# Performance work log

Measured on AMD Instinct MI355X. Metric: run time of the kernel, lower is better.

Reference implementation:

```python
import jax, jax.numpy as jnp
import numpy as np

HS = 512   # hidden_size
IN = 2048  # input_size
MB = 100   # memory_bank_size
T  = 4096  # nImg


def setup_inputs() -> dict:
    key = jax.random.key(0)
    ks = jax.random.split(key, 20)

    def w(k, i, o):
        return jax.random.normal(k, (i, o), jnp.float32) * (1.0 / np.sqrt(i))

    def b(k, o):
        return jax.random.normal(k, (o,), jnp.float32) * 0.01

    return {
        "hidden_out_a": jax.random.normal(ks[0], (T, IN), jnp.float32),
        "hidden_out_m": jax.random.normal(ks[1], (T, IN), jnp.float32),
        "W_ca": w(ks[2], HS + IN, HS),  "b_ca": b(ks[3], HS),    # hidden_to_content_a
        "W_cm": w(ks[4], HS + IN, HS),  "b_cm": b(ks[5], HS),    # hidden_to_content_m
        "W_wp": w(ks[6], 3 * HS, 3),    "b_wp": b(ks[7], 3),     # write_prob
        "W_wpa": w(ks[8], HS + IN, MB), "b_wpa": b(ks[9], MB),   # write_prob_a
        "W_wpm": w(ks[10], HS + IN, MB),"b_wpm": b(ks[11], MB),  # write_prob_m
        "W_rp": w(ks[12], 3 * HS, MB),  "b_rp": b(ks[13], MB),   # read_prob
        "W_rh": w(ks[14], 2 * HS, HS),  "b_rh": b(ks[15], HS),   # read_to_hidden
        "W_rha": w(ks[16], 2 * HS + IN, HS), "b_rha": b(ks[17], HS),  # read_to_hidden_a
        "W_rhm": w(ks[18], 2 * HS + IN, HS), "b_rhm": b(ks[19], HS),  # read_to_hidden_m
        "nImg": T,
    }


def reference(hidden_out_a, hidden_out_m,
              W_ca, b_ca, W_cm, b_cm,
              W_wp, b_wp, W_wpa, b_wpa, W_wpm, b_wpm,
              W_rp, b_rp, W_rh, b_rh,
              W_rha, b_rha, W_rhm, b_rhm,
              nImg):
    hs = W_rh.shape[1]
    mb = W_rp.shape[1]

    def step(carry, xs):
        mem, h, ha, hm = carry            # mem: [MB, HS]; h/ha/hm: [HS]
        xa, xm = xs                       # [IN] each
        xh = jnp.concatenate([ha, hm, h])               # [3*HS]
        ar = jax.nn.softmax(xh @ W_rp + b_rp)           # [MB]
        r = ar @ mem                                    # [HS] memory read
        h1 = jax.nn.relu(jnp.concatenate([r, h]) @ W_rh + b_rh)
        ha1 = jax.nn.relu(jnp.concatenate([xa, r, ha]) @ W_rha + b_rha)
        hm1 = jax.nn.relu(jnp.concatenate([xm, r, hm]) @ W_rhm + b_rhm)
        aw = jax.nn.softmax(xh @ W_wp + b_wp)           # [3] stream gate
        xha = jnp.concatenate([ha, xa])                 # [HS+IN]
        xhm = jnp.concatenate([hm, xm])
        c_a = jax.nn.relu(xha @ W_ca + b_ca)            # [HS]
        c_m = jax.nn.relu(xhm @ W_cm + b_cm)
        aw_a = jax.nn.softmax(xha @ W_wpa + b_wpa)      # [MB]
        aw_m = jax.nn.softmax(xhm @ W_wpm + b_wpm)
        mem = aw[0] * mem + aw[1] * aw_a[:, None] * c_a + aw[2] * aw_m[:, None] * c_m
        return (mem, h1, ha1, hm1), h1

    init = (jnp.zeros((mb, hs), hidden_out_a.dtype),
            jnp.zeros((hs,), hidden_out_a.dtype),
            jnp.zeros((hs,), hidden_out_a.dtype),
            jnp.zeros((hs,), hidden_out_a.dtype))
    _, hiddens = jax.lax.scan(step, init,
                              (hidden_out_a[:nImg], hidden_out_m[:nImg]))
    return hiddens  # [nImg, HS]
```

## Files before the change

kernel.cpp:

```cpp
#include <hip/hip_runtime.h>
#include <cstdint>
#include <cstddef>

#define HS 512

constexpr int TPB  = 512;
constexpr int GBLK = 64;
constexpr int OWNB = 24;

constexpr size_t OFF_TWrp  = 0;
constexpr size_t OFF_TWwp  = OFF_TWrp  + 100*1536;
constexpr size_t OFF_TWwpa = OFF_TWwp  + 3*1536;
constexpr size_t OFF_TWwpm = OFF_TWwpa + 100*512;
constexpr size_t OFF_TWca  = OFF_TWwpm + 100*512;
constexpr size_t OFF_TWcm  = OFF_TWca  + 512*512;
constexpr size_t OFF_TWh0  = OFF_TWcm  + 512*512;
constexpr size_t OFF_TWh1  = OFF_TWh0  + 512*512;
constexpr size_t OFF_TWh2  = OFF_TWh1  + 512*512;
constexpr size_t OFF_TWu0  = OFF_TWh2  + 512*512;
constexpr size_t OFF_TWu1  = OFF_TWu0  + 512*512;
constexpr size_t OFF_TWu2  = OFF_TWu1  + 512*512;
constexpr size_t OFF_PAca  = OFF_TWu2  + 512*512;
constexpr size_t OFF_PMcm  = OFF_PAca  + 4096*512;
constexpr size_t OFF_PArha = OFF_PMcm  + 4096*512;
constexpr size_t OFF_PMrhm = OFF_PArha + 4096*512;
constexpr size_t OFF_PAwpa = OFF_PMrhm + 4096*512;
constexpr size_t OFF_PMwpm = OFF_PAwpa + 4096*100;
constexpr size_t OFF_CARRY = OFF_PMwpm + 4096*100;
constexpr size_t OFF_BCAST = OFF_CARRY + 2*1536*2;

__device__ __forceinline__ unsigned long long ald(const unsigned long long* p) {
  return __hip_atomic_load(const_cast<unsigned long long*>(p),
                           __ATOMIC_RELAXED, __HIP_MEMORY_SCOPE_AGENT);
}
__device__ __forceinline__ void gstTag(unsigned long long* p, float v, unsigned tag) {
  unsigned long long u = ((unsigned long long)tag << 32) | (unsigned long long)__float_as_uint(v);
  __hip_atomic_store(p, u, __ATOMIC_RELAXED, __HIP_MEMORY_SCOPE_AGENT);
}
__device__ __forceinline__ float xrsum(float v) {
  #pragma unroll
  for (int o = 32; o; o >>= 1) v += __shfl_xor(v, o, 64);
  return v;
}
__device__ __forceinline__ float rsum16(float v) {
  #pragma unroll
  for (int o = 8; o; o >>= 1) v += __shfl_xor(v, o, 64);
  return v;
}
__device__ __forceinline__ void spinF(volatile unsigned* f, unsigned v) {
  while (*f < v) { }
  __builtin_amdgcn_sched_barrier(0);
  asm volatile("" ::: "memory");
}

__global__ void initK(unsigned long long* carryT, unsigned long long* bcast) {
  int i = blockIdx.x * blockDim.x + threadIdx.x, st = gridDim.x * blockDim.x;
  for (int k = i; k < 1536; k += st) carryT[k] = (1ull << 32);
  for (int k = i; k < 1536; k += st) carryT[1536 + k] = 0ull;
  for (int k = i; k < 2 * 1344; k += st) bcast[k] = 0ull;
}

__global__ void transK(const float* __restrict__ src, float* __restrict__ dst, int R, int C) {
  __shared__ float tile[32][33];
  int c0 = blockIdx.x * 32, r0 = blockIdx.y * 32;
  for (int i = threadIdx.y; i < 32; i += 8) {
    int r = r0 + i, c = c0 + threadIdx.x;
    tile[i][threadIdx.x] = (r < R && c < C) ? src[(size_t)r * C + c] : 0.f;
  }
  __syncthreads();
  for (int i = threadIdx.y; i < 32; i += 8) {
    int c = c0 + i, r = r0 + threadIdx.x;
    if (c < C && r < R) dst[(size_t)c * R + r] = tile[threadIdx.x][i];
  }
}

__global__ __launch_bounds__(256) void gemmK(const float* __restrict__ X,
                                             const float* __restrict__ W,
                                             float* __restrict__ C, int N) {
  __shared__ float As[16][68];
  __shared__ float Bs[16][68];
  int t0 = blockIdx.y * 64, n0 = blockIdx.x * 64;
  int tid = threadIdx.x, tx = tid & 15, ty = tid >> 4;
  float acc[4][4] = {};
  for (int k0 = 0; k0 < 2048; k0 += 16) {
    {
      int r = tid >> 2, c = (tid & 3) * 4;
      float4 v = *(const float4*)(X + (size_t)(t0 + r) * 2048 + k0 + c);
      As[c + 0][r] = v.x; As[c + 1][r] = v.y; As[c + 2][r] = v.z; As[c + 3][r] = v.w;
    }
    {
      int kr = tid >> 4, c = (tid & 15) * 4;
      int gcol = n0 + c;
      const float* src = W + (size_t)(k0 + kr) * N + gcol;
      #pragma unroll
      for (int i = 0; i < 4; ++i) Bs[kr][c + i] = (gcol + i < N) ? src[i] : 0.f;
    }
    __syncthreads();
    #pragma unroll
    for (int kk = 0; kk < 16; ++kk) {
      float4 a4 = *(const float4*)&As[kk][ty * 4];
      float4 b4 = *(const float4*)&Bs[kk][tx * 4];
      float av[4] = {a4.x, a4.y, a4.z, a4.w};
      float bv[4] = {b4.x, b4.y, b4.z, b4.w};
      #pragma unroll
      for (int i = 0; i < 4; ++i)
        #pragma unroll
        for (int j = 0; j < 4; ++j) acc[i][j] += av[i] * bv[j];
    }
    __syncthreads();
  }
  #pragma unroll
  for (int i = 0; i < 4; ++i)
    #pragma unroll
    for (int j = 0; j < 4; ++j) {
      int col = n0 + tx * 4 + j;
      if (col < N) C[(size_t)(t0 + ty * 4 + i) * N + col] = acc[i][j];
    }
}

__global__ __launch_bounds__(256) void gemm128(const float* __restrict__ X,
                                               const float* __restrict__ W,
                                               float* __restrict__ C) {
  __shared__ float As[8][132];
  __shared__ float Bs[8][132];
  const int N = 512;
  int t0 = blockIdx.y * 128, n0 = blockIdx.x * 128;
  int tid = threadIdx.x, tx = tid & 15, ty = tid >> 4;
  float acc[8][8] = {};
  for (int k0 = 0; k0 < 2048; k0 += 8) {
    int r = tid >> 1, c4 = (tid & 1) * 4;
    float4 va = *(const float4*)(X + (size_t)(t0 + r) * 2048 + k0 + c4);
    int kr = tid >> 5, cb = (tid & 31) * 4;
    float4 vb = *(const float4*)(W + (size_t)(k0 + kr) * N + n0 + cb);
    __syncthreads();
    As[c4 + 0][r] = va.x; As[c4 + 1][r] = va.y; As[c4 + 2][r] = va.z; As[c4 + 3][r] = va.w;
    Bs[kr][cb] = vb.x; Bs[kr][cb + 1] = vb.y; Bs[kr][cb + 2] = vb.z; Bs[kr][cb + 3] = vb.w;
    __syncthreads();
    #pragma unroll
    for (int kk = 0; kk < 8; ++kk) {
      float av[8], bv[8];
      *(float4*)av       = *(const float4*)&As[kk][ty * 8];
      *(float4*)(av + 4) = *(const float4*)&As[kk][ty * 8 + 4];
      *(float4*)bv       = *(const float4*)&Bs[kk][tx * 8];
      *(float4*)(bv + 4) = *(const float4*)&Bs[kk][tx * 8 + 4];
      #pragma unroll
      for (int i = 0; i < 8; ++i)
        #pragma unroll
        for (int j = 0; j < 8; ++j) acc[i][j] += av[i] * bv[j];
    }
  }
  #pragma unroll
  for (int i = 0; i < 8; ++i) {
    float* dst = C + (size_t)(t0 + ty * 8 + i) * N + n0 + tx * 8;
    *(float4*)dst       = *(float4*)&acc[i][0];
    *(float4*)(dst + 4) = *(float4*)&acc[i][4];
  }
}

struct RArgs {
  const float *TWrp, *TWwp, *TWwpa, *TWwpm, *TWca, *TWcm;
  const float *TWh0, *TWh1, *TWh2, *TWu0, *TWu1, *TWu2;
  const float *PAca, *PMcm, *PArha, *PMrhm, *PAwpa, *PMwpm;
  const float *b_ca, *b_cm, *b_wp, *b_wpa, *b_wpm, *b_rp, *b_rh, *b_rha, *b_rhm;
  unsigned long long *carryT, *bcast;
  float *out;
  int nT;
};

__global__ __launch_bounds__(TPB, 1) void recurK(RArgs a) {
  const int tid  = threadIdx.x;
  const int lane = tid & 63;
  const int lw   = tid >> 6;
  const int g    = tid >> 4;
  const int gl   = tid & 15;
  const int b    = blockIdx.x;

  __shared__ __align__(16) float s_x[1536];
  __shared__ __align__(16) float s_c[1024];
  __shared__ float s_ar[112], s_awa[112], s_awm[112], s_aw[4];
  __shared__ unsigned s_flags[8];
  volatile unsigned* FL = s_flags;

  const int r0a = (b + 51) & 63;
  const int r1m = (b + 25) & 63;
  const bool big1_grp = (b < 36);
  const bool big1_wp  = (b >= 40 && b <= 42);

  if (tid < 112) { s_ar[tid] = 0.f; s_awa[tid] = 0.f; s_awm[tid] = 0.f; }
  if (tid < 8) s_flags[tid] = 0u;

  int dstA = -1, xoffA = 0, strideA = 512;
  bool reluA = false;
  float biasA = 0.f;
  const float* preAPtr = nullptr;
  const float* wARow = nullptr;
  if (lw < 2) {
    int col = b * 8 + g;
    dstA = col; reluA = true; biasA = a.b_ca[col]; preAPtr = a.PAca + col;
    wARow = a.TWca + (size_t)col * 512; xoffA = 0;
  } else if (lw < 4) {
    int col = b * 8 + (g - 8);
    dstA = 512 + col; reluA = true; biasA = a.b_cm[col]; preAPtr = a.PMcm + col;
    wARow = a.TWcm + (size_t)col * 512; xoffA = 512;
  } else if (lw == 4) {
    int sl = g - 16;
    strideA = 100;
    if (sl == 0)                  { dstA = 1124 + r0a;      biasA = a.b_wpa[r0a];      preAPtr = a.PAwpa + r0a;      wARow = a.TWwpa + (size_t)r0a * 512;        xoffA = 0;   }
    else if (sl == 1 && r0a < 36) { dstA = 1124 + r0a + 64; biasA = a.b_wpa[r0a + 64]; preAPtr = a.PAwpa + r0a + 64; wARow = a.TWwpa + (size_t)(r0a + 64) * 512; xoffA = 0;   }
    else if (sl == 2)             { dstA = 1224 + r1m;      biasA = a.b_wpm[r1m];      preAPtr = a.PMwpm + r1m;      wARow = a.TWwpm + (size_t)r1m * 512;        xoffA = 512; }
    else if (sl == 3 && r1m < 36) { dstA = 1224 + r1m + 64; biasA = a.b_wpm[r1m + 64]; preAPtr = a.PMwpm + r1m + 64; wARow = a.TWwpm + (size_t)(r1m + 64) * 512; xoffA = 512; }
  }
  int dstBig = -1;
  float biasBig = 0.f;
  const float* wBigRow = nullptr;
  if (lw == 6) { dstBig = 1024 + b; biasBig = a.b_rp[b]; wBigRow = a.TWrp + (size_t)b * 1536; }
  else if (lw == 7) {
    if (big1_grp)      { dstBig = 1024 + b + 64;   biasBig = a.b_rp[b + 64]; wBigRow = a.TWrp + (size_t)(b + 64) * 1536; }
    else if (big1_wp)  { dstBig = 1324 + (b - 40); biasBig = a.b_wp[b - 40]; wBigRow = a.TWwp + (size_t)(b - 40) * 1536; }
  }
  const bool own = (g < OWNB);
  int ownHsel = 0, ownJ = 0, whXo = 0;
  float biasO = 0.f;
  const float* preOPtr = nullptr;
  const float* whRow = nullptr;
  const float* uRow = nullptr;
  if (own) {
    int q = b * OWNB + g, hsel = q >> 9, j = q & 511;
    ownHsel = hsel; ownJ = j;
    if (hsel == 0)      { biasO = a.b_rh[j];
                          whRow = a.TWh0 + (size_t)j * 512; whXo = 1024;
                          uRow  = a.TWu0 + (size_t)j * 512; }
    else if (hsel == 1) { biasO = a.b_rha[j]; preOPtr = a.PArha + j;
                          whRow = a.TWh1 + (size_t)j * 512; whXo = 0;
                          uRow  = a.TWu1 + (size_t)j * 512; }
    else                { biasO = a.b_rhm[j]; preOPtr = a.PMrhm + j;
                          whRow = a.TWh2 + (size_t)j * 512; whXo = 512;
                          uRow  = a.TWu2 + (size_t)j * 512; }
  }

  float4 wA[8];
  float4 wU[8];
  float4 wWh[8];
  float4 wB[6];
  float  gr[7];
  #pragma unroll
  for (int it = 0; it < 8; ++it) wA[it] = wU[it] = wWh[it] = make_float4(0.f, 0.f, 0.f, 0.f);
  #pragma unroll
  for (int it = 0; it < 6; ++it) wB[it] = make_float4(0.f, 0.f, 0.f, 0.f);
  #pragma unroll
  for (int k = 0; k < 7; ++k) gr[k] = 0.f;

  if (wARow) {
    const float4* w4 = (const float4*)wARow;
    #pragma unroll
    for (int it = 0; it < 8; ++it) wA[it] = w4[gl + 16 * it];
  }
  if (own) {
    const float4* u4 = (const float4*)uRow;
    const float4* h4 = (const float4*)whRow;
    #pragma unroll
    for (int it = 0; it < 8; ++it) { wU[it] = u4[gl + 16 * it]; wWh[it] = h4[gl + 16 * it]; }
  }
  if (wBigRow) {
    const float4* w4 = (const float4*)wBigRow;
    #pragma unroll
    for (int it = 0; it < 6; ++it) wB[it] = w4[lane + 64 * it];
  }
  __syncthreads();

  float preA_c = preAPtr ? preAPtr[0] : 0.f;
  float preO_c = preOPtr ? preOPtr[0] : 0.f;

  float whv = 0.f;
  for (int t = 0; t < a.nT; ++t) {
    const unsigned tagB = (unsigned)t + 1;
    unsigned long long* bc = a.bcast + (size_t)(t & 1) * 1344;

    {
      const unsigned long long* cin = a.carryT + (size_t)(t & 1) * 1536;
      int i0 = tid, i1 = tid + 512, i2 = tid + 1024;
      unsigned long long v0 = ald(cin + i0), v1 = ald(cin + i1), v2 = ald(cin + i2);
      while (((unsigned)(v0 >> 32) < tagB) | ((unsigned)(v1 >> 32) < tagB) |
             ((unsigned)(v2 >> 32) < tagB)) {
        __builtin_amdgcn_s_sleep(1);
        v0 = ald(cin + i0); v1 = ald(cin + i1); v2 = ald(cin + i2);
      }
      s_x[i0] = __uint_as_float((unsigned)v0);
      s_x[i1] = __uint_as_float((unsigned)v1);
      s_x[i2] = __uint_as_float((unsigned)v2);
    }
    __syncthreads();

    const int tn = (t + 1 < a.nT) ? t + 1 : t;
    float preA_n = preAPtr ? preAPtr[(size_t)tn * strideA] : 0.f;
    float preO_n = preOPtr ? preOPtr[(size_t)tn * 512] : 0.f;

    if (dstA >= 0) {
      const float4* x4 = (const float4*)(s_x + xoffA);
      float acc = 0.f;
      #pragma unroll
      for (int it = 0; it < 8; ++it) {
        float4 xv = x4[gl + 16 * it];
        acc += wA[it].x * xv.x + wA[it].y * xv.y + wA[it].z * xv.z + wA[it].w * xv.w;
      }
      float v = rsum16(acc);
      if (!gl) {
        v += preA_c + biasA;
        if (reluA) v = fmaxf(v, 0.f);
        gstTag(bc + dstA, v, tagB);
      }
    } else if (dstBig >= 0) {
      const float4* x4 = (const float4*)s_x;
      float acc = 0.f;
      #pragma unroll
      for (int it = 0; it < 6; ++it) {
        float4 xv = x4[lane + 64 * it];
        acc += wB[it].x * xv.x + wB[it].y * xv.y + wB[it].z * xv.z + wB[it].w * xv.w;
      }
      float v = xrsum(acc);
      if (!lane) gstTag(bc + dstBig, v + biasBig, tagB);
    }
    if (own) {
      const float4* x4 = (const float4*)(s_x + whXo);
      float acc = 0.f;
      #pragma unroll
      for (int it = 0; it < 8; ++it) {
        float4 xv = x4[gl + 16 * it];
        acc += wWh[it].x * xv.x + wWh[it].y * xv.y + wWh[it].z * xv.z + wWh[it].w * xv.w;
      }
      whv = rsum16(acc);
    }

    if (lw == 0) {
      const unsigned long long* p1 = bc + 1024 + lane;
      bool two = lane < 36;
      bool wpx = (lane >= 40 && lane < 43);
      const unsigned long long* pw = bc + 1324 + (lane - 40);
      unsigned long long v1 = ald(p1);
      unsigned long long v2 = two ? ald(p1 + 64) : ~0ull;
      unsigned long long vw = wpx ? ald(pw) : ~0ull;
      while (((unsigned)(v1 >> 32) < tagB) | ((unsigned)(v2 >> 32) < tagB) |
             ((unsigned)(vw >> 32) < tagB)) {
        __builtin_amdgcn_s_sleep(1);
        v1 = ald(p1); if (two) v2 = ald(p1 + 64); if (wpx) vw = ald(pw);
      }
      float x1 = __uint_as_float((unsigned)v1);
      float x2 = two ? __uint_as_float((unsigned)v2) : -3.0e38f;
      float m = fmaxf(x1, x2);
      #pragma unroll
      for (int o = 32; o; o >>= 1) m = fmaxf(m, __shfl_xor(m, o, 64));
      float e1 = expf(x1 - m);
      float e2 = two ? expf(x2 - m) : 0.f;
      float ss = e1 + e2;
      #pragma unroll
      for (int o = 32; o; o >>= 1) ss += __shfl_xor(ss, o, 64);
      float inv = 1.f / ss;
      s_ar[lane] = e1 * inv;
      if (two) s_ar[64 + lane] = e2 * inv;
      asm volatile("s_waitcnt lgkmcnt(0)" ::: "memory");
      if (!lane) FL[0] = tagB;
    }

    unsigned long long* cout = a.carryT + (size_t)((t + 1) & 1) * 1536;
    if (own) {
      spinF(&FL[0], tagB);
      float contrib = 0.f;
      #pragma unroll
      for (int k = 0; k < 7; ++k) contrib += s_ar[gl + 16 * k] * gr[k];
      contrib = rsum16(contrib);
      if (!gl) {
        float h = fmaxf(contrib + whv + preO_c + biasO, 0.f);
        if (ownHsel == 0) {
          a.out[(size_t)t * 512 + ownJ] = h;
          gstTag(cout + 1024 + ownJ, h, tagB + 1);
        } else if (ownHsel == 1) {
          gstTag(cout + ownJ, h, tagB + 1);
        } else {
          gstTag(cout + 512 + ownJ, h, tagB + 1);
        }
      }
    }

    if (lw == 1) {
      const unsigned long long* p1 = bc + 1124 + lane;
      bool two = lane < 36;
      unsigned long long v1 = ald(p1);
      unsigned long long v2 = two ? ald(p1 + 64) : ~0ull;
      while (((unsigned)(v1 >> 32) < tagB) | ((unsigned)(v2 >> 32) < tagB)) {
        __builtin_amdgcn_s_sleep(1);
        v1 = ald(p1); if (two) v2 = ald(p1 + 64);
      }
      float x1 = __uint_as_float((unsigned)v1);
      float x2 = two ? __uint_as_float((unsigned)v2) : -3.0e38f;
      float m = fmaxf(x1, x2);
      #pragma unroll
      for (int o = 32; o; o >>= 1) m = fmaxf(m, __shfl_xor(m, o, 64));
      float e1 = expf(x1 - m);
      float e2 = two ? expf(x2 - m) : 0.f;
      float ss = e1 + e2;
      #pragma unroll
      for (int o = 32; o; o >>= 1) ss += __shfl_xor(ss, o, 64);
      float inv = 1.f / ss;
      s_awa[lane] = e1 * inv;
      if (two) s_awa[64 + lane] = e2 * inv;
      asm volatile("s_waitcnt lgkmcnt(0)" ::: "memory");
      if (!lane) FL[2] = tagB;
    } else if (lw == 2) {
      const unsigned long long* p1 = bc + 1224 + lane;
      bool two = lane < 36;
      unsigned long long v1 = ald(p1);
      unsigned long long v2 = two ? ald(p1 + 64) : ~0ull;
      while (((unsigned)(v1 >> 32) < tagB) | ((unsigned)(v2 >> 32) < tagB)) {
        __builtin_amdgcn_s_sleep(1);
        v1 = ald(p1); if (two) v2 = ald(p1 + 64);
      }
      float x1 = __uint_as_float((unsigned)v1);
      float x2 = two ? __uint_as_float((unsigned)v2) : -3.0e38f;
      float m = fmaxf(x1, x2);
      #pragma unroll
      for (int o = 32; o; o >>= 1) m = fmaxf(m, __shfl_xor(m, o, 64));
      float e1 = expf(x1 - m);
      float e2 = two ? expf(x2 - m) : 0.f;
      float ss = e1 + e2;
      #pragma unroll
      for (int o = 32; o; o >>= 1) ss += __shfl_xor(ss, o, 64);
      float inv = 1.f / ss;
      s_awm[lane] = e1 * inv;
      if (two) s_awm[64 + lane] = e2 * inv;
      asm volatile("s_waitcnt lgkmcnt(0)" ::: "memory");
      if (!lane) FL[3] = tagB;
    } else if (lw == 3) {
      float x = -3.0e38f;
      if (lane < 3) {
        const unsigned long long* p = bc + 1324 + lane;
        unsigned long long v = ald(p);
        while ((unsigned)(v >> 32) < tagB) { __builtin_amdgcn_s_sleep(1); v = ald(p); }
        x = __uint_as_float((unsigned)v);
      }
      float m = x;
      #pragma unroll
      for (int o = 32; o; o >>= 1) m = fmaxf(m, __shfl_xor(m, o, 64));
      float e = (lane < 3) ? expf(x - m) : 0.f;
      float ss = e;
      #pragma unroll
      for (int o = 32; o; o >>= 1) ss += __shfl_xor(ss, o, 64);
      if (lane < 3) s_aw[lane] = e / ss;
      asm volatile("s_waitcnt lgkmcnt(0)" ::: "memory");
      if (!lane) FL[1] = tagB;
    } else if (lw >= 6) {
      int ci = tid - 384;
      const unsigned long long* p = bc + ci;
      unsigned long long v[8];
      #pragma unroll
      for (int k = 0; k < 8; ++k) v[k] = ald(p + 128 * k);
      for (;;) {
        bool ok = true;
        #pragma unroll
        for (int k = 0; k < 8; ++k) ok &= ((unsigned)(v[k] >> 32) >= tagB);
        if (__all(ok)) break;
        __builtin_amdgcn_s_sleep(1);
        #pragma unroll
        for (int k = 0; k < 8; ++k) v[k] = ald(p + 128 * k);
      }
      #pragma unroll
      for (int k = 0; k < 8; ++k) s_c[ci + 128 * k] = __uint_as_float((unsigned)v[k]);
      asm volatile("s_waitcnt lgkmcnt(0)" ::: "memory");
      if (!lane) FL[4 + (lw - 6)] = tagB;
    }

    if (own) {
      spinF(&FL[4], tagB);
      spinF(&FL[5], tagB);
      const float4* a4 = (const float4*)s_c;
      const float4* m4 = (const float4*)(s_c + 512);
      float sa = 0.f, sm = 0.f;
      #pragma unroll
      for (int it = 0; it < 8; ++it) {
        float4 av = a4[gl + 16 * it], mv = m4[gl + 16 * it];
        sa += wU[it].x * av.x + wU[it].y * av.y + wU[it].z * av.z + wU[it].w * av.w;
        sm += wU[it].x * mv.x + wU[it].y * mv.y + wU[it].z * mv.z + wU[it].w * mv.w;
      }
      #pragma unroll
      for (int o = 8; o; o >>= 1) { sa += __shfl_xor(sa, o, 64); sm += __shfl_xor(sm, o, 64); }
      const float uA = sa, uM = sm;

      spinF(&FL[1], tagB);
      spinF(&FL[2], tagB);
      spinF(&FL[3], tagB);
      const float aw0 = s_aw[0], aw1 = s_aw[1], aw2 = s_aw[2];
      #pragma unroll
      for (int k = 0; k < 7; ++k) {
        int idx = gl + 16 * k;
        gr[k] = aw0 * gr[k] + aw1 * s_awa[idx] * uA + aw2 * s_awm[idx] * uM;
      }
    }

    preA_c = preA_n;
    preO_c = preO_n;
  }
}

extern "C" void kernel_launch(void* const* d_in, const int* in_sizes, int n_in,
                              void* d_out, int out_size, void* d_ws, size_t ws_size,
                              hipStream_t stream) {
  const float* Xa    = (const float*)d_in[0];
  const float* Xm    = (const float*)d_in[1];
  const float* W_ca  = (const float*)d_in[2];  const float* b_ca  = (const float*)d_in[3];
  const float* W_cm  = (const float*)d_in[4];  const float* b_cm  = (const float*)d_in[5];
  const float* W_wp  = (const float*)d_in[6];  const float* b_wp  = (const float*)d_in[7];
  const float* W_wpa = (const float*)d_in[8];  const float* b_wpa = (const float*)d_in[9];
  const float* W_wpm = (const float*)d_in[10]; const float* b_wpm = (const float*)d_in[11];
  const float* W_rp  = (const float*)d_in[12]; const float* b_rp  = (const float*)d_in[13];
  const float* W_rh  = (const float*)d_in[14]; const float* b_rh  = (const float*)d_in[15];
  const float* W_rha = (const float*)d_in[16]; const float* b_rha = (const float*)d_in[17];
  const float* W_rhm = (const float*)d_in[18]; const float* b_rhm = (const float*)d_in[19];

  int nT = out_size / HS;
  float* ws = (float*)d_ws;

  initK<<<dim3(64), dim3(256), 0, stream>>>(
      (unsigned long long*)(ws + OFF_CARRY),
      (unsigned long long*)(ws + OFF_BCAST));

  dim3 tb(32, 8);
  auto tg = [](int R, int C) { return dim3((C + 31) / 32, (R + 31) / 32); };
  transK<<<tg(1536, 100), tb, 0, stream>>>(W_rp,                       ws + OFF_TWrp,  1536, 100);
  transK<<<tg(1536, 3),   tb, 0, stream>>>(W_wp,                       ws + OFF_TWwp,  1536, 3);
  transK<<<tg(512, 100),  tb, 0, stream>>>(W_wpa,                      ws + OFF_TWwpa, 512, 100);
  transK<<<tg(512, 100),  tb, 0, stream>>>(W_wpm,                      ws + OFF_TWwpm, 512, 100);
  transK<<<tg(512, 512),  tb, 0, stream>>>(W_ca,                       ws + OFF_TWca,  512, 512);
  transK<<<tg(512, 512),  tb, 0, stream>>>(W_cm,                       ws + OFF_TWcm,  512, 512);
  transK<<<tg(512, 512),  tb, 0, stream>>>(W_rh  + 512 * 512,          ws + OFF_TWh0,  512, 512);
  transK<<<tg(512, 512),  tb, 0, stream>>>(W_rha + (size_t)2560 * 512, ws + OFF_TWh1,  512, 512);
  transK<<<tg(512, 512),  tb, 0, stream>>>(W_rhm + (size_t)2560 * 512, ws + OFF_TWh2,  512, 512);
  transK<<<tg(512, 512),  tb, 0, stream>>>(W_rh,                       ws + OFF_TWu0,  512, 512);
  transK<<<tg(512, 512),  tb, 0, stream>>>(W_rha + (size_t)2048 * 512, ws + OFF_TWu1,  512, 512);
  transK<<<tg(512, 512),  tb, 0, stream>>>(W_rhm + (size_t)2048 * 512, ws + OFF_TWu2,  512, 512);

  int tB = nT / 128;
  gemm128<<<dim3(4, tB), dim3(256), 0, stream>>>(Xa, W_ca + (size_t)512 * 512, ws + OFF_PAca);
  gemm128<<<dim3(4, tB), dim3(256), 0, stream>>>(Xm, W_cm + (size_t)512 * 512, ws + OFF_PMcm);
  gemm128<<<dim3(4, tB), dim3(256), 0, stream>>>(Xa, W_rha,                    ws + OFF_PArha);
  gemm128<<<dim3(4, tB), dim3(256), 0, stream>>>(Xm, W_rhm,                    ws + OFF_PMrhm);
  int tB64 = nT / 64;
  gemmK<<<dim3(2, tB64), dim3(256), 0, stream>>>(Xa, W_wpa + (size_t)512 * 100, ws + OFF_PAwpa, 100);
  gemmK<<<dim3(2, tB64), dim3(256), 0, stream>>>(Xm, W_wpm + (size_t)512 * 100, ws + OFF_PMwpm, 100);

  RArgs a;
  a.TWrp  = ws + OFF_TWrp;  a.TWwp  = ws + OFF_TWwp;
  a.TWwpa = ws + OFF_TWwpa; a.TWwpm = ws + OFF_TWwpm;
  a.TWca  = ws + OFF_TWca;  a.TWcm  = ws + OFF_TWcm;
  a.TWh0  = ws + OFF_TWh0;  a.TWh1  = ws + OFF_TWh1;  a.TWh2 = ws + OFF_TWh2;
  a.TWu0  = ws + OFF_TWu0;  a.TWu1  = ws + OFF_TWu1;  a.TWu2 = ws + OFF_TWu2;
  a.PAca  = ws + OFF_PAca;  a.PMcm  = ws + OFF_PMcm;
  a.PArha = ws + OFF_PArha; a.PMrhm = ws + OFF_PMrhm;
  a.PAwpa = ws + OFF_PAwpa; a.PMwpm = ws + OFF_PMwpm;
  a.b_ca = b_ca; a.b_cm = b_cm; a.b_wp = b_wp; a.b_wpa = b_wpa; a.b_wpm = b_wpm;
  a.b_rp = b_rp; a.b_rh = b_rh; a.b_rha = b_rha; a.b_rhm = b_rhm;
  a.carryT = (unsigned long long*)(ws + OFF_CARRY);
  a.bcast  = (unsigned long long*)(ws + OFF_BCAST);
  a.out    = (float*)d_out;
  a.nT     = nT;

  recurK<<<dim3(GBLK), dim3(TPB), 0, stream>>>(a);
}
```

Before: 25.28 ms.

## Replace LDS flag spin-waits with block barriers and remap wave roles

Removes the per-wave shared-memory flag handshakes (spinF on FL[]) and replaces them with two __syncthreads per step. The three softmax computations are consolidated into wave 0 and the content-vector gather into wave 1. Owner groups move to g>=8 and the content-column work is redistributed across the remaining groups. This removes LDS spin polling and frees waves 6-7 from gather duty, but it serialises softmax work in one wave and forces every wave to wait at full-block barriers.

```diff
diff --git a/kernel.cpp b/kernel.cpp
--- a/kernel.cpp
+++ b/kernel.cpp
@@ -47,11 +47,6 @@
   for (int o = 8; o; o >>= 1) v += __shfl_xor(v, o, 64);
   return v;
 }
-__device__ __forceinline__ void spinF(volatile unsigned* f, unsigned v) {
-  while (*f < v) { }
-  __builtin_amdgcn_sched_barrier(0);
-  asm volatile("" ::: "memory");
-}
 
 __global__ void initK(unsigned long long* carryT, unsigned long long* bcast) {
   int i = blockIdx.x * blockDim.x + threadIdx.x, st = gridDim.x * blockDim.x;
@@ -178,8 +173,6 @@
   __shared__ __align__(16) float s_x[1536];
   __shared__ __align__(16) float s_c[1024];
   __shared__ float s_ar[112], s_awa[112], s_awm[112], s_aw[4];
-  __shared__ unsigned s_flags[8];
-  volatile unsigned* FL = s_flags;
 
   const int r0a = (b + 51) & 63;
   const int r1m = (b + 25) & 63;
@@ -187,22 +180,26 @@
   const bool big1_wp  = (b >= 40 && b <= 42);
 
   if (tid < 112) { s_ar[tid] = 0.f; s_awa[tid] = 0.f; s_awm[tid] = 0.f; }
-  if (tid < 8) s_flags[tid] = 0u;
+  if (tid < 4) s_aw[tid] = 0.f;
 
   int dstA = -1, xoffA = 0, strideA = 512;
   bool reluA = false;
   float biasA = 0.f;
   const float* preAPtr = nullptr;
   const float* wARow = nullptr;
-  if (lw < 2) {
-    int col = b * 8 + g;
+  if (g >= 4 && g < 8) {
+    int col = b * 8 + (g - 4);
     dstA = col; reluA = true; biasA = a.b_ca[col]; preAPtr = a.PAca + col;
     wARow = a.TWca + (size_t)col * 512; xoffA = 0;
-  } else if (lw < 4) {
+  } else if (g >= 20 && g < 24) {
+    int col = b * 8 + (g - 16);
+    dstA = col; reluA = true; biasA = a.b_ca[col]; preAPtr = a.PAca + col;
+    wARow = a.TWca + (size_t)col * 512; xoffA = 0;
+  } else if (g >= 8 && g < 16) {
     int col = b * 8 + (g - 8);
     dstA = 512 + col; reluA = true; biasA = a.b_cm[col]; preAPtr = a.PMcm + col;
     wARow = a.TWcm + (size_t)col * 512; xoffA = 512;
-  } else if (lw == 4) {
+  } else if (g >= 16 && g < 20) {
     int sl = g - 16;
     strideA = 100;
     if (sl == 0)                  { dstA = 1124 + r0a;      biasA = a.b_wpa[r0a];      preAPtr = a.PAwpa + r0a;      wARow = a.TWwpa + (size_t)r0a * 512;        xoffA = 0;   }
@@ -218,14 +215,16 @@
     if (big1_grp)      { dstBig = 1024 + b + 64;   biasBig = a.b_rp[b + 64]; wBigRow = a.TWrp + (size_t)(b + 64) * 1536; }
     else if (big1_wp)  { dstBig = 1324 + (b - 40); biasBig = a.b_wp[b - 40]; wBigRow = a.TWwp + (size_t)(b - 40) * 1536; }
   }
-  const bool own = (g < OWNB);
-  int ownHsel = 0, ownJ = 0, whXo = 0;
+  const bool own = (g >= 8);
+  const int rr = g - 8;
+  int ownHsel = 0, ownJ = 0, whXo = 0, qOwn = 0;
   float biasO = 0.f;
   const float* preOPtr = nullptr;
   const float* whRow = nullptr;
   const float* uRow = nullptr;
   if (own) {
-    int q = b * OWNB + g, hsel = q >> 9, j = q & 511;
+    qOwn = b * OWNB + rr;
+    int hsel = qOwn >> 9, j = qOwn & 511;
     ownHsel = hsel; ownJ = j;
     if (hsel == 0)      { biasO = a.b_rh[j];
                           whRow = a.TWh0 + (size_t)j * 512; whXo = 1024;
@@ -271,7 +270,6 @@
   float preA_c = preAPtr ? preAPtr[0] : 0.f;
   float preO_c = preOPtr ? preOPtr[0] : 0.f;
 
-  float whv = 0.f;
   for (int t = 0; t < a.nT; ++t) {
     const unsigned tagB = (unsigned)t + 1;
     unsigned long long* bc = a.bcast + (size_t)(t & 1) * 1344;
@@ -320,6 +318,7 @@
       float v = xrsum(acc);
       if (!lane) gstTag(bc + dstBig, v + biasBig, tagB);
     }
+    float whv = 0.f;
     if (own) {
       const float4* x4 = (const float4*)(s_x + whXo);
       float acc = 0.f;
@@ -334,15 +333,11 @@
     if (lw == 0) {
       const unsigned long long* p1 = bc + 1024 + lane;
       bool two = lane < 36;
-      bool wpx = (lane >= 40 && lane < 43);
-      const unsigned long long* pw = bc + 1324 + (lane - 40);
       unsigned long long v1 = ald(p1);
       unsigned long long v2 = two ? ald(p1 + 64) : ~0ull;
-      unsigned long long vw = wpx ? ald(pw) : ~0ull;
-      while (((unsigned)(v1 >> 32) < tagB) | ((unsigned)(v2 >> 32) < tagB) |
-             ((unsigned)(vw >> 32) < tagB)) {
+      while (((unsigned)(v1 >> 32) < tagB) | ((unsigned)(v2 >> 32) < tagB)) {
         __builtin_amdgcn_s_sleep(1);
-        v1 = ald(p1); if (two) v2 = ald(p1 + 64); if (wpx) vw = ald(pw);
+        v1 = ald(p1); if (two) v2 = ald(p1 + 64);
       }
       float x1 = __uint_as_float((unsigned)v1);
       float x2 = two ? __uint_as_float((unsigned)v2) : -3.0e38f;
@@ -357,13 +352,11 @@
       float inv = 1.f / ss;
       s_ar[lane] = e1 * inv;
       if (two) s_ar[64 + lane] = e2 * inv;
-      asm volatile("s_waitcnt lgkmcnt(0)" ::: "memory");
-      if (!lane) FL[0] = tagB;
-    }
+    }
+    __syncthreads();
 
     unsigned long long* cout = a.carryT + (size_t)((t + 1) & 1) * 1536;
     if (own) {
-      spinF(&FL[0], tagB);
       float contrib = 0.f;
       #pragma unroll
       for (int k = 0; k < 7; ++k) contrib += s_ar[gl + 16 * k] * gr[k];
@@ -381,96 +374,84 @@
       }
     }
 
-    if (lw == 1) {
-      const unsigned long long* p1 = bc + 1124 + lane;
-      bool two = lane < 36;
-      unsigned long long v1 = ald(p1);
-      unsigned long long v2 = two ? ald(p1 + 64) : ~0ull;
-      while (((unsigned)(v1 >> 32) < tagB) | ((unsigned)(v2 >> 32) < tagB)) {
+    if (lw == 0) {
+      bool two = lane < 36, wpx = lane < 3;
+      const unsigned long long* pa = bc + 1124 + lane;
+      const unsigned long long* pm = bc + 1224 + lane;
+      const unsigned long long* pw = bc + 1324 + lane;
+      unsigned long long a1 = ald(pa), m1 = ald(pm);
+      unsigned long long a2 = two ? ald(pa + 64) : ~0ull;
+      unsigned long long m2 = two ? ald(pm + 64) : ~0ull;
+      unsigned long long w1 = wpx ? ald(pw) : ~0ull;
+      while (((unsigned)(a1 >> 32) < tagB) | ((unsigned)(a2 >> 32) < tagB) |
+             ((unsigned)(m1 >> 32) < tagB) | ((unsigned)(m2 >> 32) < tagB) |
+             ((unsigned)(w1 >> 32) < tagB)) {
         __builtin_amdgcn_s_sleep(1);
-        v1 = ald(p1); if (two) v2 = ald(p1 + 64);
-      }
-      float x1 = __uint_as_float((unsigned)v1);
-      float x2 = two ? __uint_as_float((unsigned)v2) : -3.0e38f;
-      float m = fmaxf(x1, x2);
-      #pragma unroll
-      for (int o = 32; o; o >>= 1) m = fmaxf(m, __shfl_xor(m, o, 64));
-      float e1 = expf(x1 - m);
-      float e2 = two ? expf(x2 - m) : 0.f;
-      float ss = e1 + e2;
-      #pragma unroll
-      for (int o = 32; o; o >>= 1) ss += __shfl_xor(ss, o, 64);
-      float inv = 1.f / ss;
-      s_awa[lane] = e1 * inv;
-      if (two) s_awa[64 + lane] = e2 * inv;
-      asm volatile("s_waitcnt lgkmcnt(0)" ::: "memory");
-      if (!lane) FL[2] = tagB;
-    } else if (lw == 2) {
-      const unsigned long long* p1 = bc + 1224 + lane;
-      bool two = lane < 36;
-      unsigned long long v1 = ald(p1);
-      unsigned long long v2 = two ? ald(p1 + 64) : ~0ull;
-      while (((unsigned)(v1 >> 32) < tagB) | ((unsigned)(v2 >> 32) < tagB)) {
-        __builtin_amdgcn_s_sleep(1);
-        v1 = ald(p1); if (two) v2 = ald(p1 + 64);
-      }
-      float x1 = __uint_as_float((unsigned)v1);
-      float x2 = two ? __uint_as_float((unsigned)v2) : -3.0e38f;
-      float m = fmaxf(x1, x2);
-      #pragma unroll
-      for (int o = 32; o; o >>= 1) m = fmaxf(m, __shfl_xor(m, o, 64));
-      float e1 = expf(x1 - m);
-      float e2 = two ? expf(x2 - m) : 0.f;
-      float ss = e1 + e2;
-      #pragma unroll
-      for (int o = 32; o; o >>= 1) ss += __shfl_xor(ss, o, 64);
-      float inv = 1.f / ss;
-      s_awm[lane] = e1 * inv;
-      if (two) s_awm[64 + lane] = e2 * inv;
-      asm volatile("s_waitcnt lgkmcnt(0)" ::: "memory");
-      if (!lane) FL[3] = tagB;
-    } else if (lw == 3) {
-      float x = -3.0e38f;
-      if (lane < 3) {
-        const unsigned long long* p = bc + 1324 + lane;
-        unsigned long long v = ald(p);
-        while ((unsigned)(v >> 32) < tagB) { __builtin_amdgcn_s_sleep(1); v = ald(p); }
-        x = __uint_as_float((unsigned)v);
-      }
-      float m = x;
-      #pragma unroll
-      for (int o = 32; o; o >>= 1) m = fmaxf(m, __shfl_xor(m, o, 64));
-      float e = (lane < 3) ? expf(x - m) : 0.f;
-      float ss = e;
-      #pragma unroll
-      for (int o = 32; o; o >>= 1) ss += __shfl_xor(ss, o, 64);
-      if (lane < 3) s_aw[lane] = e / ss;
-      asm volatile("s_waitcnt lgkmcnt(0)" ::: "memory");
-      if (!lane) FL[1] = tagB;
-    } else if (lw >= 6) {
-      int ci = tid - 384;
-      const unsigned long long* p = bc + ci;
-      unsigned long long v[8];
-      #pragma unroll
-      for (int k = 0; k < 8; ++k) v[k] = ald(p + 128 * k);
+        a1 = ald(pa); m1 = ald(pm);
+        if (two) { a2 = ald(pa + 64); m2 = ald(pm + 64); }
+        if (wpx) w1 = ald(pw);
+      }
+      {
+        float x1 = __uint_as_float((unsigned)a1);
+        float x2 = two ? __uint_as_float((unsigned)a2) : -3.0e38f;
+        float m = fmaxf(x1, x2);
+        #pragma unroll
+        for (int o = 32; o; o >>= 1) m = fmaxf(m, __shfl_xor(m, o, 64));
+        float e1 = expf(x1 - m);
+        float e2 = two ? expf(x2 - m) : 0.f;
+        float ss = e1 + e2;
+        #pragma unroll
+        for (int o = 32; o; o >>= 1) ss += __shfl_xor(ss, o, 64);
+        float inv = 1.f / ss;
+        s_awa[lane] = e1 * inv;
+        if (two) s_awa[64 + lane] = e2 * inv;
+      }
+      {
+        float x1 = __uint_as_float((unsigned)m1);
+        float x2 = two ? __uint_as_float((unsigned)m2) : -3.0e38f;
+        float m = fmaxf(x1, x2);
+        #pragma unroll
+        for (int o = 32; o; o >>= 1) m = fmaxf(m, __shfl_xor(m, o, 64));
+        float e1 = expf(x1 - m);
+        float e2 = two ? expf(x2 - m) : 0.f;
+        float ss = e1 + e2;
+        #pragma unroll
+        for (int o = 32; o; o >>= 1) ss += __shfl_xor(ss, o, 64);
+        float inv = 1.f / ss;
+        s_awm[lane] = e1 * inv;
+        if (two) s_awm[64 + lane] = e2 * inv;
+      }
+      {
+        float x = wpx ? __uint_as_float((unsigned)w1) : -3.0e38f;
+        float m = x;
+        #pragma unroll
+        for (int o = 32; o; o >>= 1) m = fmaxf(m, __shfl_xor(m, o, 64));
+        float e = wpx ? expf(x - m) : 0.f;
+        float ss = e;
+        #pragma unroll
+        for (int o = 32; o; o >>= 1) ss += __shfl_xor(ss, o, 64);
+        if (wpx) s_aw[lane] = e / ss;
+      }
+    } else if (lw == 1) {
+      const unsigned long long* p = bc + lane;
+      unsigned long long v[16];
+      #pragma unroll
+      for (int k = 0; k < 16; ++k) v[k] = ald(p + 64 * k);
       for (;;) {
         bool ok = true;
         #pragma unroll
-        for (int k = 0; k < 8; ++k) ok &= ((unsigned)(v[k] >> 32) >= tagB);
+        for (int k = 0; k < 16; ++k) ok &= ((unsigned)(v[k] >> 32) >= tagB);
         if (__all(ok)) break;
         __builtin_amdgcn_s_sleep(1);
         #pragma unroll
-        for (int k = 0; k < 8; ++k) v[k] = ald(p + 128 * k);
-      }
-      #pragma unroll
-      for (int k = 0; k < 8; ++k) s_c[ci + 128 * k] = __uint_as_float((unsigned)v[k]);
-      asm volatile("s_waitcnt lgkmcnt(0)" ::: "memory");
-      if (!lane) FL[4 + (lw - 6)] = tagB;
-    }
+        for (int k = 0; k < 16; ++k) v[k] = ald(p + 64 * k);
+      }
+      #pragma unroll
+      for (int k = 0; k < 16; ++k) s_c[lane + 64 * k] = __uint_as_float((unsigned)v[k]);
+    }
+    __syncthreads();
 
     if (own) {
-      spinF(&FL[4], tagB);
-      spinF(&FL[5], tagB);
       const float4* a4 = (const float4*)s_c;
       const float4* m4 = (const float4*)(s_c + 512);
       float sa = 0.f, sm = 0.f;
@@ -483,10 +464,6 @@
       #pragma unroll
       for (int o = 8; o; o >>= 1) { sa += __shfl_xor(sa, o, 64); sm += __shfl_xor(sm, o, 64); }
       const float uA = sa, uM = sm;
-
-      spinF(&FL[1], tagB);
-      spinF(&FL[2], tagB);
-      spinF(&FL[3], tagB);
       const float aw0 = s_aw[0], aw1 = s_aw[1], aw2 = s_aw[2];
       #pragma unroll
       for (int k = 0; k < 7; ++k) {
```

Result: slower. 27.47 ms (+8.7%).
